# Kernel optimization log

Measured on AMD Instinct MI355X. Metric: run time of the kernel, lower is better.

Reference implementation:

```python
import itertools
import jax, jax.numpy as jnp
import numpy as np

ALPHA = 1e-4   # mse/conn mixing
BETA = 0.1
DMAX = 20.0
NCAP = 10.0    # costs_n_cap
PCAP = 3.0     # costs_p_cap
W3D = 64       # 3D cube window (window_3d)
W2D = 32       # 2D MALIS window (window_2d, default)


def _dilate5(mask):
    # scipy binary_dilation, default cross structuring element, 5 iterations
    m = mask.astype(bool)
    for _ in range(5):
        p = np.pad(m, 1)
        m = p[1:-1, 1:-1] | p[:-2, 1:-1] | p[2:, 1:-1] | p[1:-1, :-2] | p[1:-1, 2:]
    return m


def _label8(mask):
    # skimage.measure.label on boolean mask: 8-connectivity, background=0
    H, W = mask.shape
    lbl = np.zeros((H, W), np.int64)
    parent = {}

    def find(x):
        while parent[x] != x:
            parent[x] = parent[parent[x]]
            x = parent[x]
        return x

    nxt = 1
    for i in range(H):
        for j in range(W):
            if not mask[i, j]:
                continue
            neigh = []
            for di, dj in ((-1, -1), (-1, 0), (-1, 1), (0, -1)):
                ii, jj = i + di, j + dj
                if 0 <= ii < H and 0 <= jj < W and mask[ii, jj]:
                    neigh.append(int(lbl[ii, jj]))
            if not neigh:
                lbl[i, j] = nxt
                parent[nxt] = nxt
                nxt += 1
            else:
                m0 = min(neigh)
                lbl[i, j] = m0
                for nb in neigh:
                    ra, rb = find(m0), find(nb)
                    if ra != rb:
                        parent[max(ra, rb)] = min(ra, rb)
    out = np.zeros_like(lbl)
    remap = {}
    c = 0
    for i in range(H):
        for j in range(W):
            if lbl[i, j] > 0:
                r = find(int(lbl[i, j]))
                if r not in remap:
                    c += 1
                    remap[r] = c
                out[i, j] = remap[r]
    return out


def _malis_edge_weights(seg, n1, n2, costs, pos):
    # MALIS union-find / Kruskal maximal-spanning-tree pair counting.
    # Edges processed in descending cost order. Background (seg==0) nodes
    # are not counted. pos=1: #same-label pairs merged; pos=0: #diff-label pairs.
    n = seg.size
    parent = list(range(n))

    def find(x):
        r = x
        while parent[r] != r:
            r = parent[r]
        while parent[x] != r:
            parent[x], x = r, parent[x]
        return r

    cnt = [({int(s): 1} if s > 0 else {}) for s in seg]
    tot = [1 if s > 0 else 0 for s in seg]
    w = np.zeros(costs.shape[0], np.float32)
    for e in np.argsort(-costs, kind="stable"):
        ra, rb = find(int(n1[e])), find(int(n2[e]))
        if ra == rb:
            continue
        ca, cb = cnt[ra], cnt[rb]
        if len(ca) > len(cb):
            ra, rb, ca, cb = rb, ra, cb, ca
        same = 0
        for l, v in ca.items():
            same += v * cb.get(l, 0)
        w[e] = float(same if pos else tot[ra] * tot[rb] - same)
        for l, v in ca.items():
            cb[l] = cb.get(l, 0) + v
        tot[rb] += tot[ra]
        parent[ra] = rb
        cnt[ra] = None
    return w


def _window_weights(pred2d, tgt2d):
    # numpy MALIS node weights for a [B,1,H,W] 2D projection
    B, C, H, W = pred2d.shape
    w = W2D
    wn = np.zeros(pred2d.shape, np.float32)
    wp = np.zeros(pred2d.shape, np.float32)
    idx = np.arange(w * w).reshape(w, w)
    n1 = np.concatenate([idx[:, :-1].ravel(), idx[:-1, :].ravel()])
    n2 = np.concatenate([idx[:, 1:].ravel(), idx[1:, :].ravel()])
    nh = w * (w - 1)
    for k in range(H // w):
        for j in range(W // w):
            p = pred2d[:, :, k*w:(k+1)*w, j*w:(j+1)*w]
            t = tgt2d[:, :, k*w:(k+1)*w, j*w:(j+1)*w]
            ch = (p[:, :, :, :-1] + p[:, :, :, 1:]).reshape(B, -1)
            cv = (p[:, :, :-1, :] + p[:, :, 1:, :]).reshape(B, -1)
            costs = np.concatenate([ch, cv], 1).astype(np.float32)
            gh = (t[:, :, :, :-1] + t[:, :, :, 1:]).reshape(B, -1)
            gv = (t[:, :, :-1, :] + t[:, :, 1:, :]).reshape(B, -1)
            gt = np.concatenate([gh, gv], 1).astype(np.float32)
            costs_n = costs.copy()
            costs_p = costs.copy()
            costs_n[gt > NCAP] = NCAP
            costs_p[gt < PCAP] = 0.0
            gt = np.minimum(gt, NCAP)
            for b in range(B):
                sg = _label8(~_dilate5(t[b, 0] == 0)).ravel()
                en = _malis_edge_weights(sg, n1, n2, costs_n[b], 0)
                ep = _malis_edge_weights(sg, n1, n2, costs_p[b], 1)
                sn = en.sum()
                if sn > 0:
                    en = en / sn
                sp = ep.sum()
                if sp > 0:
                    ep = ep / sp
                en[gt[b] >= PCAP] = 0.0
                ep[gt[b] < NCAP] = 0.0
                for ew, out in ((en, wn), (ep, wp)):
                    eh = ew[:nh].reshape(w, w - 1)
                    ev = ew[nh:].reshape(w - 1, w)
                    nwt = np.zeros((w, w), np.float32)
                    nwt[:, :-1] += eh
                    nwt[:, 1:] += eh
                    nwt[:-1, :] += ev
                    nwt[1:, :] += ev
                    out[b, 0, k*w:(k+1)*w, j*w:(j+1)*w] = nwt
    return wn, wp


def _precompute(pred_np, tgt_np):
    # host-side (detached) MALIS weight maps, exactly as the torch module
    B, C, H, W, D = pred_np.shape
    items = []
    for k, j, i in itertools.product(range(H // W3D), range(W // W3D), range(D // W3D)):
        sl = (slice(None), slice(None), slice(k*W3D, (k+1)*W3D),
              slice(j*W3D, (j+1)*W3D), slice(i*W3D, (i+1)*W3D))
        pc, tc = pred_np[sl], tgt_np[sl]
        for axis in (2, 3, 4):
            wn, wp = _window_weights(pc.min(axis=axis), tc.min(axis=axis))
            items.append((k, j, i, axis, jnp.asarray(wn), jnp.asarray(wp)))
    return items


def _loss(pred, target, items):
    mse = jnp.mean((pred - target) ** 2)
    conn = jnp.float32(0.0)
    for (k, j, i, axis, wn, wp) in items:
        pc = pred[:, :, k*W3D:(k+1)*W3D, j*W3D:(j+1)*W3D, i*W3D:(i+1)*W3D]
        proj = jnp.min(pc, axis=axis)  # [B,1,64,64]
        conn = conn + jnp.sum(proj**2 * wn + BETA * (DMAX - proj)**2 * wp)
    return (mse, jnp.float32(ALPHA) * conn)


def setup_inputs() -> dict:
    # synthetic distance-transform-like volumes (zeros on 'vessel' seeds)
    rng = np.random.default_rng(0)
    B, H = 4, 128
    g = np.arange(H, dtype=np.float32)
    zz, yy, xx = np.meshgrid(g, g, g, indexing="ij")
    tgt = np.empty((B, 1, H, H, H), np.float32)
    for b in range(B):
        pts = rng.uniform(0, H, size=(24, 3)).astype(np.float32)
        d = np.full((H, H, H), np.inf, np.float32)
        for p in pts:
            d = np.minimum(d, np.sqrt((zz - p[0])**2 + (yy - p[1])**2 + (xx - p[2])**2))
        tgt[b, 0] = np.floor(np.minimum(d, DMAX))
    pred = np.clip(tgt + 0.5 * rng.standard_normal(tgt.shape).astype(np.float32), 0.0, DMAX).astype(np.float32)
    return {"pred": jnp.asarray(pred), "target": jnp.asarray(tgt)}


def reference(pred, target):
    items = _precompute(np.asarray(pred), np.asarray(target))
    return _loss(pred, target, items)
```

## Files before the change

### kernel.cpp

```cpp
#include <hip/hip_runtime.h>

#define BLOCK 256
#define NNODE 1024
#define NH    992
#define NE    1984
#define NSORT 2048
#define LMAX  12
#define CHUNK 64
#define NPASS (NE / CHUNK)

typedef unsigned long long ull;

__device__ __forceinline__ void edge_nodes(int e, int& a, int& b) {
    if (e < NH) {
        int r = e / 31;
        int c = e - r * 31;
        a = (r << 5) + c;
        b = a + 1;
    } else {
        a = e - NH;
        b = a + 32;
    }
}

__device__ __forceinline__ int find_par(unsigned short* par, int x) {
    volatile unsigned short* vp = par;
    int r = x;
    int p = vp[r];
    while (p != r) { r = p; p = vp[r]; }
    int c = x;
    while (c != r) { const int nxt = vp[c]; vp[c] = (unsigned short)r; c = nxt; }
    return r;
}

__device__ __forceinline__ int dot16x4(ull a, ull b) {
    int s  = (int)(a & 0xFFFFu)         * (int)(b & 0xFFFFu);
    s     += (int)((a >> 16) & 0xFFFFu) * (int)((b >> 16) & 0xFFFFu);
    s     += (int)((a >> 32) & 0xFFFFu) * (int)((b >> 32) & 0xFFFFu);
    s     += (int)((a >> 48) & 0xFFFFu) * (int)((b >> 48) & 0xFFFFu);
    return s;
}

__device__ __forceinline__ void cswap(unsigned int& ka, unsigned short& ia,
                                      unsigned int& kb, unsigned short& ib, bool up) {
    const bool gt = (ka > kb) || (ka == kb && ia > ib);
    if (gt == up) {
        const unsigned int  tk = ka; ka = kb; kb = tk;
        const unsigned short ti = ia; ia = ib; ib = ti;
    }
}

__global__ __launch_bounds__(BLOCK) void prep_kernel(const float* __restrict__ pred,
                                                     const float* __restrict__ tgt,
                                                     char* __restrict__ ws,
                                                     int B) {
    __shared__ alignas(16) float sh_p[NNODE];
    __shared__ alignas(16) float sh_t[NNODE];
    __shared__ unsigned char  mA[NNODE];
    __shared__ unsigned char  mB[NNODE];
    __shared__ unsigned short sh_parent[NNODE];
    __shared__ unsigned short sh_lab[NNODE];
    __shared__ int sh_flag;
    __shared__ int sh_L;

    const int tid = threadIdx.x;
    const int w = blockIdx.x;
    int wg = w;
    const int b    = wg % B;  wg /= B;
    const int win  = wg & 3;  wg >>= 2;
    const int item = wg;
    const int axis_id = item % 3;
    const int cube = item / 3;
    const int ci = cube & 1;
    const int cj = (cube >> 1) & 1;
    const int ck = (cube >> 2) & 1;
    const int wk = win >> 1;
    const int wj = win & 1;

    const int NW = 96 * B;
    float* Pb = (float*)(ws + 64);
    float* Tb = Pb + (size_t)NW * NNODE;
    unsigned char* Sb = (unsigned char*)(Tb + (size_t)NW * NNODE);
    int* Lb = (int*)(Sb + (size_t)NW * NNODE);

    const size_t base = (size_t)b * 2097152u;

    if (axis_id == 2) {
        for (int pix = tid; pix < NNODE; pix += BLOCK) {
            const int r = pix >> 5, c = pix & 31;
            const int R = wk * 32 + r, C = wj * 32 + c;
            const size_t idx0 = base + (size_t)(ck * 64 + R) * 16384u + (size_t)(cj * 64 + C) * 128u + (size_t)(ci * 64);
            const float4* pp = reinterpret_cast<const float4*>(pred + idx0);
            const float4* tp = reinterpret_cast<const float4*>(tgt + idx0);
            float pm = 3.4e38f, tm = 3.4e38f;
            #pragma unroll
            for (int h = 0; h < 16; ++h) {
                const float4 a = pp[h];
                const float4 t = tp[h];
                pm = fminf(pm, fminf(fminf(a.x, a.y), fminf(a.z, a.w)));
                tm = fminf(tm, fminf(fminf(t.x, t.y), fminf(t.z, t.w)));
            }
            sh_p[pix] = pm;
            sh_t[pix] = tm;
        }
    } else {
        const int r  = tid >> 3;
        const int c0 = (tid & 7) << 2;
        const int R = wk * 32 + r, C = wj * 32 + c0;
        size_t idx0; int hstride;
        if (axis_id == 0) {
            idx0 = base + (size_t)(ck * 64) * 16384u + (size_t)(cj * 64 + R) * 128u + (size_t)(ci * 64 + C);
            hstride = 16384;
        } else {
            idx0 = base + (size_t)(ck * 64 + R) * 16384u + (size_t)(cj * 64) * 128u + (size_t)(ci * 64 + C);
            hstride = 128;
        }
        float4 pm = make_float4(3.4e38f, 3.4e38f, 3.4e38f, 3.4e38f);
        float4 tm = pm;
        #pragma unroll 8
        for (int h = 0; h < 64; ++h) {
            const float4 a  = *reinterpret_cast<const float4*>(pred + idx0);
            const float4 t4 = *reinterpret_cast<const float4*>(tgt + idx0);
            pm.x = fminf(pm.x, a.x);  pm.y = fminf(pm.y, a.y);
            pm.z = fminf(pm.z, a.z);  pm.w = fminf(pm.w, a.w);
            tm.x = fminf(tm.x, t4.x); tm.y = fminf(tm.y, t4.y);
            tm.z = fminf(tm.z, t4.z); tm.w = fminf(tm.w, t4.w);
            idx0 += (size_t)hstride;
        }
        *reinterpret_cast<float4*>(&sh_p[(r << 5) + c0]) = pm;
        *reinterpret_cast<float4*>(&sh_t[(r << 5) + c0]) = tm;
    }
    __syncthreads();

    for (int pix = tid; pix < NNODE; pix += BLOCK)
        mA[pix] = (sh_t[pix] == 0.0f) ? 1 : 0;
    __syncthreads();
    for (int it = 0; it < 5; ++it) {
        unsigned char* src = (it & 1) ? mB : mA;
        unsigned char* dst = (it & 1) ? mA : mB;
        for (int pix = tid; pix < NNODE; pix += BLOCK) {
            const int r = pix >> 5, c = pix & 31;
            unsigned char v = src[pix];
            if (r > 0)  v |= src[pix - 32];
            if (r < 31) v |= src[pix + 32];
            if (c > 0)  v |= src[pix - 1];
            if (c < 31) v |= src[pix + 1];
            dst[pix] = v;
        }
        __syncthreads();
    }
    for (int pix = tid; pix < NNODE; pix += BLOCK)
        mA[pix] = mB[pix] ^ 1;
    __syncthreads();

    for (int pix = tid; pix < NNODE; pix += BLOCK)
        sh_parent[pix] = mA[pix] ? (unsigned short)pix : (unsigned short)0xFFFF;
    __syncthreads();
    for (;;) {
        if (tid == 0) sh_flag = 0;
        __syncthreads();
        for (int pix = tid; pix < NNODE; pix += BLOCK) {
            if (!mA[pix]) continue;
            const int r = pix >> 5, c = pix & 31;
            int m = sh_parent[pix];
            #pragma unroll
// ... 57 lines not shown
    __shared__ unsigned short sh_parent[NNODE];
    __shared__ unsigned int   sh_szto[NNODE];
    __shared__ ull            sh_cnt64[NNODE * 3];
    __shared__ alignas(16) unsigned char sh_seg[NNODE];
    __shared__ float          sh_sn;
    __shared__ double         sh_red[4];

    const int tid = threadIdx.x;
    int wg = blockIdx.x;
    const int sign = wg & 1;  wg >>= 1;
    const int w = wg;

    const int NW = 96 * B;
    const float* Pb = (const float*)(ws_c + 64);
    const float* Tb = Pb + (size_t)NW * NNODE;
    const unsigned char* Sb = (const unsigned char*)(Tb + (size_t)NW * NNODE);
    const int* Lb = (const int*)(Sb + (size_t)NW * NNODE);

    const int Lraw = Lb[w];
    if (Lraw == 0 || (Lraw == 1 && sign == 0)) return;
    const int mode = (Lraw <= 1) ? 0 : ((Lraw <= 4) ? 1 : 2);

    {
        const int p4 = tid << 2;
        *reinterpret_cast<float4*>(&sh_p[p4]) =
            *reinterpret_cast<const float4*>(&Pb[(size_t)w * NNODE + p4]);
        *reinterpret_cast<float4*>(&sh_t[p4]) =
            *reinterpret_cast<const float4*>(&Tb[(size_t)w * NNODE + p4]);
        ((unsigned int*)sh_seg)[tid] =
            ((const unsigned int*)Sb)[(size_t)w * (NNODE / 4) + tid];
    }
    __syncthreads();

    for (int pix = tid; pix < NNODE; pix += BLOCK) {
        sh_parent[pix] = (unsigned short)pix;
        const int s = sh_seg[pix];
        const unsigned int tot = (s > 0 && s <= LMAX) ? 1u : 0u;
        sh_szto[pix] = 1u | (tot << 16);
        if (mode >= 1) {
            ull c0 = 0, c1 = 0, c2 = 0;
            if (s >= 1 && s <= LMAX) {
                const ull bit = 1ull << (((s - 1) & 3) * 16);
                const int q = (s - 1) >> 2;
                if (q == 0) c0 = bit; else if (q == 1) c1 = bit; else c2 = bit;
            }
            sh_cnt64[pix * 3 + 0] = c0;
            if (mode == 2) {
                sh_cnt64[pix * 3 + 1] = c1;
                sh_cnt64[pix * 3 + 2] = c2;
            }
        }
    }
    __syncthreads();

    unsigned int   K[8];
    unsigned short I[8];
    const int b8 = tid << 3;
    #pragma unroll
    for (int l = 0; l < 8; ++l) {
        const int e = b8 + l;
        if (e < NE) {
            int a, bb; edge_nodes(e, a, bb);
            float cost = sh_p[a] + sh_p[bb];
            const float g = sh_t[a] + sh_t[bb];
            if (sign == 0) { if (g > 10.0f) cost = 10.0f; }
            else           { if (g <  3.0f) cost = 0.0f;  }
            K[l] = ~__float_as_uint(cost);
            I[l] = (unsigned short)e;
        } else {
            K[l] = 0xFFFFFFFFu;
            I[l] = (unsigned short)0xFFFF;
        }
    }
    cswap(K[0],I[0],K[1],I[1], true );
    cswap(K[2],I[2],K[3],I[3], false);
    cswap(K[4],I[4],K[5],I[5], true );
    cswap(K[6],I[6],K[7],I[7], false);
    cswap(K[0],I[0],K[2],I[2], true );
    cswap(K[1],I[1],K[3],I[3], true );
    cswap(K[4],I[4],K[6],I[6], false);
    cswap(K[5],I[5],K[7],I[7], false);
    cswap(K[0],I[0],K[1],I[1], true );
    cswap(K[2],I[2],K[3],I[3], true );
    cswap(K[4],I[4],K[5],I[5], false);
    cswap(K[6],I[6],K[7],I[7], false);
// ... 41 lines not shown
            const uint4 k1 = *reinterpret_cast<const uint4*>(&sh_key[b8 + 4]);
            const uint4 iv = *reinterpret_cast<const uint4*>(&sh_idx[b8]);
            K[0]=k0.x; K[1]=k0.y; K[2]=k0.z; K[3]=k0.w;
            K[4]=k1.x; K[5]=k1.y; K[6]=k1.z; K[7]=k1.w;
            I[0]=(unsigned short)(iv.x); I[1]=(unsigned short)(iv.x>>16);
            I[2]=(unsigned short)(iv.y); I[3]=(unsigned short)(iv.y>>16);
            I[4]=(unsigned short)(iv.z); I[5]=(unsigned short)(iv.z>>16);
            I[6]=(unsigned short)(iv.w); I[7]=(unsigned short)(iv.w>>16);
            const bool u8 = ((b8 & k) == 0);
            cswap(K[0],I[0],K[4],I[4], u8); cswap(K[1],I[1],K[5],I[5], u8);
            cswap(K[2],I[2],K[6],I[6], u8); cswap(K[3],I[3],K[7],I[7], u8);
            cswap(K[0],I[0],K[2],I[2], u8); cswap(K[1],I[1],K[3],I[3], u8);
            cswap(K[4],I[4],K[6],I[6], u8); cswap(K[5],I[5],K[7],I[7], u8);
            cswap(K[0],I[0],K[1],I[1], u8); cswap(K[2],I[2],K[3],I[3], u8);
            cswap(K[4],I[4],K[5],I[5], u8); cswap(K[6],I[6],K[7],I[7], u8);
            uint4 o0, o1, ov;
            o0.x=K[0]; o0.y=K[1]; o0.z=K[2]; o0.w=K[3];
            o1.x=K[4]; o1.y=K[5]; o1.z=K[6]; o1.w=K[7];
            ov.x=(unsigned int)I[0] | ((unsigned int)I[1]<<16);
            ov.y=(unsigned int)I[2] | ((unsigned int)I[3]<<16);
            ov.z=(unsigned int)I[4] | ((unsigned int)I[5]<<16);
            ov.w=(unsigned int)I[6] | ((unsigned int)I[7]<<16);
            *reinterpret_cast<uint4*>(&sh_key[b8])     = o0;
            *reinterpret_cast<uint4*>(&sh_key[b8 + 4]) = o1;
            *reinterpret_cast<uint4*>(&sh_idx[b8])     = ov;
        }
        __syncthreads();
    }

    for (int e = tid; e < NE; e += BLOCK) sh_key[e] = 0u;
    __syncthreads();

    if (tid < 64) {
        const int lane = tid;
        for (int pass = 0; pass < NPASS; ++pass) {
            const int e = sh_idx[pass * CHUNK + lane];
            int a, bb; edge_nodes(e, a, bb);
            int ra = find_par(sh_parent, a);
            int rb = find_par(sh_parent, bb);
            ull m = __ballot(ra != rb);
            while (m) {
                const int i = (int)__builtin_ctzll(m);
                m &= m - 1;
                const unsigned int pack = (unsigned int)ra | ((unsigned int)rb << 10) | ((unsigned int)e << 20);
                const unsigned int pk = (unsigned int)__shfl((int)pack, i);
                const int ra_i = (int)(pk & 1023u);
                const int rb_i = (int)((pk >> 10) & 1023u);
                if (ra_i == rb_i) continue;
                const int se = (int)(pk >> 20);
                const unsigned int xa = sh_szto[ra_i], xb = sh_szto[rb_i];
                const int ta = (int)(xa >> 16), tb = (int)(xb >> 16);
                const int big = ((xa & 0xFFFFu) > (xb & 0xFFFFu));
                const int rs = big ? ra_i : rb_i;
                const int rl = big ? rb_i : ra_i;
                int wv;
                if (mode == 0) {
                    wv = ta * tb;
                } else if (mode == 1) {
                    const ull a0 = sh_cnt64[ra_i * 3];
                    const ull b0 = sh_cnt64[rb_i * 3];
                    const int same = dot16x4(a0, b0);
                    wv = sign ? same : (ta * tb - same);
                    if (lane == 0 && (ta + tb) > 0)
                        sh_cnt64[rs * 3] = a0 + b0;
                } else {
                    const ull a0 = sh_cnt64[ra_i * 3 + 0];
                    const ull a1 = sh_cnt64[ra_i * 3 + 1];
                    const ull a2 = sh_cnt64[ra_i * 3 + 2];
                    const ull b0 = sh_cnt64[rb_i * 3 + 0];
                    const ull b1 = sh_cnt64[rb_i * 3 + 1];
                    const ull b2 = sh_cnt64[rb_i * 3 + 2];
                    const int same = dot16x4(a0, b0) + dot16x4(a1, b1) + dot16x4(a2, b2);
                    wv = sign ? same : (ta * tb - same);
                    if (lane == 0 && (ta + tb) > 0) {
                        sh_cnt64[rs * 3 + 0] = a0 + b0;
                        sh_cnt64[rs * 3 + 1] = a1 + b1;
                        sh_cnt64[rs * 3 + 2] = a2 + b2;
                    }
                }
                if (lane == 0) {
                    sh_key[se] = __float_as_uint((float)wv);
                    sh_szto[rs] = xa + xb;
                    sh_parent[rl] = (unsigned short)rs;
                }
                if (ra == rl) ra = rs;
                if (rb == rl) rb = rs;
            }
        }
    }
    __syncthreads();

    {
        float part = 0.0f;
        for (int e = tid; e < NE; e += BLOCK) part += __uint_as_float(sh_key[e]);
        for (int off = 32; off > 0; off >>= 1) part += __shfl_down(part, off, 64);
        if ((tid & 63) == 0) sh_red[tid >> 6] = (double)part;
        __syncthreads();
        if (tid == 0) sh_sn = (float)(sh_red[0] + sh_red[1] + sh_red[2] + sh_red[3]);
        __syncthreads();
    }
    const float sn = sh_sn;

    double acc = 0.0;
    for (int pix = tid; pix < NNODE; pix += BLOCK) {
        const int r = pix >> 5, c = pix & 31;
        float nw = 0.0f;
        if (c < 31) { const int e = r * 31 + c;
            float v = __uint_as_float(sh_key[e]); if (sn > 0.0f) v = v / sn;
            const float g = sh_t[pix] + sh_t[pix + 1];
            if (sign == 0) { if (g >= 3.0f) v = 0.0f; } else { if (g < 10.0f) v = 0.0f; }
            nw += v; }
        if (c > 0)  { const int e = r * 31 + c - 1;
            float v = __uint_as_float(sh_key[e]); if (sn > 0.0f) v = v / sn;
            const float g = sh_t[pix - 1] + sh_t[pix];
            if (sign == 0) { if (g >= 3.0f) v = 0.0f; } else { if (g < 10.0f) v = 0.0f; }
            nw += v; }
        if (r < 31) { const int e = NH + pix;
            float v = __uint_as_float(sh_key[e]); if (sn > 0.0f) v = v / sn;
            const float g = sh_t[pix] + sh_t[pix + 32];
            if (sign == 0) { if (g >= 3.0f) v = 0.0f; } else { if (g < 10.0f) v = 0.0f; }
            nw += v; }
// ... 143 lines not shown
        }
        __syncthreads();
        const int f = sh_flag;
        __syncthreads();
        if (f == 0) break;
    }

    if (tid == 0) sh_L = 0;
    __syncthreads();
    for (int pix = tid; pix < NNODE; pix += BLOCK) {
        if (mA[pix] && (int)sh_parent[pix] == pix) {
            const int id = atomicAdd(&sh_L, 1);
            sh_szto[pix] = (unsigned int)(id + 1);
        }
    }
    __syncthreads();
    for (int pix = tid; pix < NNODE; pix += BLOCK) {
        unsigned char s = 0;
        if (mA[pix]) {
            int lab = (int)sh_szto[sh_parent[pix]];
            if (lab > 255) lab = 255;
            s = (unsigned char)lab;
        }
        sh_seg[pix] = s;
    }
    __syncthreads();

    const int Lraw = sh_L;
    const int mode = (Lraw <= 1) ? 0 : ((Lraw <= 4) ? 1 : 2);
    const bool skip_all = (Lraw == 0) || (Lraw == 1 && sign == 0);

    if (!skip_all) {

    for (int pix = tid; pix < NNODE; pix += BLOCK) {
        sh_parent[pix] = (unsigned short)pix;
        const int s = sh_seg[pix];
        const unsigned int tot = (s > 0 && s <= LMAX) ? 1u : 0u;
        sh_szto[pix] = 1u | (tot << 16);
        if (mode >= 1) {
            ull c0 = 0, c1 = 0, c2 = 0;
            if (s >= 1 && s <= LMAX) {
                const ull bit = 1ull << (((s - 1) & 3) * 16);
                const int q = (s - 1) >> 2;
                if (q == 0) c0 = bit; else if (q == 1) c1 = bit; else c2 = bit;
            }
            sh_cnt64[pix * 3 + 0] = c0;
            if (mode == 2) {
                sh_cnt64[pix * 3 + 1] = c1;
                sh_cnt64[pix * 3 + 2] = c2;
            }
        }
    }
    __syncthreads();

    unsigned int   K[8];
    unsigned short I[8];
    const int b8 = tid << 3;
    #pragma unroll
    for (int l = 0; l < 8; ++l) {
        const int e = b8 + l;
        if (e < NE) {
            int a, bb; edge_nodes(e, a, bb);
            float cost = sh_p[a] + sh_p[bb];
            const float g = sh_t[a] + sh_t[bb];
            if (sign == 0) { if (g > 10.0f) cost = 10.0f; }
            else           { if (g <  3.0f) cost = 0.0f;  }
            K[l] = ~__float_as_uint(cost);
            I[l] = (unsigned short)e;
        } else {
            K[l] = 0xFFFFFFFFu;
            I[l] = (unsigned short)0xFFFF;
        }
    }
    cswap(K[0],I[0],K[1],I[1], true );
    cswap(K[2],I[2],K[3],I[3], false);
    cswap(K[4],I[4],K[5],I[5], true );
    cswap(K[6],I[6],K[7],I[7], false);
    cswap(K[0],I[0],K[2],I[2], true );
    cswap(K[1],I[1],K[3],I[3], true );
    cswap(K[4],I[4],K[6],I[6], false);
    cswap(K[5],I[5],K[7],I[7], false);
    cswap(K[0],I[0],K[1],I[1], true );
    cswap(K[2],I[2],K[3],I[3], true );
    cswap(K[4],I[4],K[5],I[5], false);
    cswap(K[6],I[6],K[7],I[7], false);
// ... 41 lines not shown
            const uint4 k1 = *reinterpret_cast<const uint4*>(&sh_key[b8 + 4]);
            const uint4 iv = *reinterpret_cast<const uint4*>(&sh_idx[b8]);
            K[0]=k0.x; K[1]=k0.y; K[2]=k0.z; K[3]=k0.w;
            K[4]=k1.x; K[5]=k1.y; K[6]=k1.z; K[7]=k1.w;
            I[0]=(unsigned short)(iv.x); I[1]=(unsigned short)(iv.x>>16);
            I[2]=(unsigned short)(iv.y); I[3]=(unsigned short)(iv.y>>16);
            I[4]=(unsigned short)(iv.z); I[5]=(unsigned short)(iv.z>>16);
            I[6]=(unsigned short)(iv.w); I[7]=(unsigned short)(iv.w>>16);
            const bool u8 = ((b8 & k) == 0);
            cswap(K[0],I[0],K[4],I[4], u8); cswap(K[1],I[1],K[5],I[5], u8);
            cswap(K[2],I[2],K[6],I[6], u8); cswap(K[3],I[3],K[7],I[7], u8);
            cswap(K[0],I[0],K[2],I[2], u8); cswap(K[1],I[1],K[3],I[3], u8);
            cswap(K[4],I[4],K[6],I[6], u8); cswap(K[5],I[5],K[7],I[7], u8);
            cswap(K[0],I[0],K[1],I[1], u8); cswap(K[2],I[2],K[3],I[3], u8);
            cswap(K[4],I[4],K[5],I[5], u8); cswap(K[6],I[6],K[7],I[7], u8);
            uint4 o0, o1, ov;
            o0.x=K[0]; o0.y=K[1]; o0.z=K[2]; o0.w=K[3];
            o1.x=K[4]; o1.y=K[5]; o1.z=K[6]; o1.w=K[7];
            ov.x=(unsigned int)I[0] | ((unsigned int)I[1]<<16);
            ov.y=(unsigned int)I[2] | ((unsigned int)I[3]<<16);
            ov.z=(unsigned int)I[4] | ((unsigned int)I[5]<<16);
            ov.w=(unsigned int)I[6] | ((unsigned int)I[7]<<16);
            *reinterpret_cast<uint4*>(&sh_key[b8])     = o0;
            *reinterpret_cast<uint4*>(&sh_key[b8 + 4]) = o1;
            *reinterpret_cast<uint4*>(&sh_idx[b8])     = ov;
        }
        __syncthreads();
    }

    for (int e = tid; e < NE; e += BLOCK) sh_key[e] = 0u;
    __syncthreads();

    if (tid < 64) {
        const int lane = tid;
        for (int pass = 0; pass < NPASS; ++pass) {
            const int e = sh_idx[pass * CHUNK + lane];
            int a, bb; edge_nodes(e, a, bb);
            int ra = find_par(sh_parent, a);
            int rb = find_par(sh_parent, bb);
            ull m = __ballot(ra != rb);
            while (m) {
                const int i = (int)__builtin_ctzll(m);
                m &= m - 1;
                const unsigned int pack = (unsigned int)ra | ((unsigned int)rb << 10) | ((unsigned int)e << 20);
                const unsigned int pk = (unsigned int)__shfl((int)pack, i);
                const int ra_i = (int)(pk & 1023u);
                const int rb_i = (int)((pk >> 10) & 1023u);
                if (ra_i == rb_i) continue;
                const int se = (int)(pk >> 20);
                const unsigned int xa = sh_szto[ra_i], xb = sh_szto[rb_i];
                const int ta = (int)(xa >> 16), tb = (int)(xb >> 16);
                const int big = ((xa & 0xFFFFu) > (xb & 0xFFFFu));
                const int rs = big ? ra_i : rb_i;
                const int rl = big ? rb_i : ra_i;
                int wv;
                if (mode == 0) {
                    wv = ta * tb;
                } else if (mode == 1) {
                    const ull a0 = sh_cnt64[ra_i * 3];
                    const ull b0 = sh_cnt64[rb_i * 3];
                    const int same = dot16x4(a0, b0);
                    wv = sign ? same : (ta * tb - same);
                    if (lane == 0 && (ta + tb) > 0)
                        sh_cnt64[rs * 3] = a0 + b0;
                } else {
                    const ull a0 = sh_cnt64[ra_i * 3 + 0];
                    const ull a1 = sh_cnt64[ra_i * 3 + 1];
                    const ull a2 = sh_cnt64[ra_i * 3 + 2];
                    const ull b0 = sh_cnt64[rb_i * 3 + 0];
                    const ull b1 = sh_cnt64[rb_i * 3 + 1];
                    const ull b2 = sh_cnt64[rb_i * 3 + 2];
                    const int same = dot16x4(a0, b0) + dot16x4(a1, b1) + dot16x4(a2, b2);
                    wv = sign ? same : (ta * tb - same);
                    if (lane == 0 && (ta + tb) > 0) {
                        sh_cnt64[rs * 3 + 0] = a0 + b0;
                        sh_cnt64[rs * 3 + 1] = a1 + b1;
                        sh_cnt64[rs * 3 + 2] = a2 + b2;
                    }
                }
                if (lane == 0) {
                    sh_key[se] = __float_as_uint((float)wv);
                    sh_szto[rs] = xa + xb;
                    sh_parent[rl] = (unsigned short)rs;
                }
                if (ra == rl) ra = rs;
                if (rb == rl) rb = rs;
            }
        }
    }
    __syncthreads();

    {
        float part = 0.0f;
        for (int e = tid; e < NE; e += BLOCK) part += __uint_as_float(sh_key[e]);
        for (int off = 32; off > 0; off >>= 1) part += __shfl_down(part, off, 64);
        if ((tid & 63) == 0) sh_red[tid >> 6] = (double)part;
        __syncthreads();
        if (tid == 0) sh_sn = (float)(sh_red[0] + sh_red[1] + sh_red[2] + sh_red[3]);
        __syncthreads();
    }
    const float sn = sh_sn;

    double acc = 0.0;
    for (int pix = tid; pix < NNODE; pix += BLOCK) {
        const int r = pix >> 5, c = pix & 31;
        float nw = 0.0f;
        if (c < 31) { const int e = r * 31 + c;
            float v = __uint_as_float(sh_key[e]); if (sn > 0.0f) v = v / sn;
            const float g = sh_t[pix] + sh_t[pix + 1];
            if (sign == 0) { if (g >= 3.0f) v = 0.0f; } else { if (g < 10.0f) v = 0.0f; }
            nw += v; }
        if (c > 0)  { const int e = r * 31 + c - 1;
            float v = __uint_as_float(sh_key[e]); if (sn > 0.0f) v = v / sn;
            const float g = sh_t[pix - 1] + sh_t[pix];
            if (sign == 0) { if (g >= 3.0f) v = 0.0f; } else { if (g < 10.0f) v = 0.0f; }
            nw += v; }
        if (r < 31) { const int e = NH + pix;
            float v = __uint_as_float(sh_key[e]); if (sn > 0.0f) v = v / sn;
            const float g = sh_t[pix] + sh_t[pix + 32];
            if (sign == 0) { if (g >= 3.0f) v = 0.0f; } else { if (g < 10.0f) v = 0.0f; }
            nw += v; }
// ... 25 lines not shown
    for (long i = (long)blockIdx.x * BLOCK + threadIdx.x; i < n; i += (long)gridDim.x * BLOCK) {
        const float d = pred[i] - tgt[i];
        acc += (double)(d * d);
    }
    for (int off = 32; off > 0; off >>= 1) acc += __shfl_down(acc, off, 64);
    __shared__ double red[4];
    if ((threadIdx.x & 63) == 0) red[threadIdx.x >> 6] = acc;
    __syncthreads();
    if (threadIdx.x == 0)
        atomicAdd(&acc_ws[0], red[0] + red[1] + red[2] + red[3]);
}

__global__ void fin_kernel(const double* __restrict__ acc_ws, float* __restrict__ out, long n) {
    if (threadIdx.x == 0 && blockIdx.x == 0) {
        out[0] = (float)(acc_ws[0] / (double)n);
        out[1] = (float)(acc_ws[1] * (double)1e-4f);
    }
}

extern "C" void kernel_launch(void* const* d_in, const int* in_sizes, int n_in,
                              void* d_out, int out_size, void* d_ws, size_t ws_size,
                              hipStream_t stream) {
    const float* pred = (const float*)d_in[0];
    const float* tgt  = (const float*)d_in[1];
    float* out = (float*)d_out;
    double* acc = (double*)d_ws;

    const long n = (long)in_sizes[0];
    const int  B = (int)(n / 2097152);
    const int  NW = 96 * B;
    const size_t need = 64 + (size_t)NW * NNODE * 9 + (size_t)NW * 4;

    hipMemsetAsync(d_ws, 0, 2 * sizeof(double), stream);
    mse_kernel<<<1024, BLOCK, 0, stream>>>(pred, tgt, acc, n);
    if (ws_size >= need) {
        prep_kernel<<<NW, BLOCK, 0, stream>>>(pred, tgt, (char*)d_ws, B);
        solve_kernel<<<192 * B, BLOCK, 0, stream>>>((const char*)d_ws, acc, B);
    } else {
        conn_kernel<<<192 * B, BLOCK, 0, stream>>>(pred, tgt, acc, B);
    }
    fin_kernel<<<1, 64, 0, stream>>>(acc, out, n);
}
```

Measured before the change: 539.3 us.

## Forward component state in registers through serial Kruskal merges, specialize by mode

Each candidate lane now loads its roots' size and label-count vectors up front. The serial merge loop then passes these values by shuffle and updates them in registers after each merge, so it no longer reads shared memory on the critical path. The next candidate is prefetched while the current one is processed, and the code is templated on mode to remove runtime branches. The cost is more register pressure, more shuffles, and trickier logic for keeping root ids and forwarded data consistent.

Result: slower. 593.7 us (+10.1%).

```diff
diff --git a/kernel.cpp b/kernel.cpp
--- a/kernel.cpp
+++ b/kernel.cpp
@@ -41,12 +41,124 @@
     return s;
 }
 
+__device__ __forceinline__ ull shfl64(ull v, int src) {
+    const int lo = __shfl((int)(unsigned int)(v & 0xFFFFFFFFu), src);
+    const int hi = __shfl((int)(unsigned int)(v >> 32), src);
+    return ((ull)(unsigned int)hi << 32) | (ull)(unsigned int)lo;
+}
+
 __device__ __forceinline__ void cswap(unsigned int& ka, unsigned short& ia,
                                       unsigned int& kb, unsigned short& ib, bool up) {
     const bool gt = (ka > kb) || (ka == kb && ia > ib);
     if (gt == up) {
         const unsigned int  tk = ka; ka = kb; kb = tk;
         const unsigned short ti = ia; ia = ib; ib = ti;
+    }
+}
+
+template<int MODE>
+__device__ __forceinline__ void kruskal_run(unsigned short* sh_parent,
+                                            unsigned int*   sh_szto,
+                                            ull*            sh_cnt64,
+                                            unsigned int*   sh_key,
+                                            const unsigned short* sh_idx,
+                                            const int sign, const int lane) {
+    for (int pass = 0; pass < NPASS; ++pass) {
+        const int e = sh_idx[pass * CHUNK + lane];
+        int a, bb; edge_nodes(e, a, bb);
+        int ra = find_par(sh_parent, a);
+        int rb = find_par(sh_parent, bb);
+        unsigned int xa = 0, xb = 0;
+        ull a0 = 0, a1 = 0, a2 = 0, b0 = 0, b1 = 0, b2 = 0;
+        const bool cand = (ra != rb);
+        if (cand) {
+            xa = sh_szto[ra]; xb = sh_szto[rb];
+            if (MODE >= 1) { a0 = sh_cnt64[ra * 3]; b0 = sh_cnt64[rb * 3]; }
+            if (MODE == 2) {
+                a1 = sh_cnt64[ra * 3 + 1]; a2 = sh_cnt64[ra * 3 + 2];
+                b1 = sh_cnt64[rb * 3 + 1]; b2 = sh_cnt64[rb * 3 + 2];
+            }
+        }
+        ull m = __ballot(cand);
+        if (m == 0) continue;
+
+        {
+            const int i0 = (int)__builtin_ctzll(m); m &= m - 1;
+            unsigned int pk  = (unsigned int)__shfl(
+                (int)((unsigned int)ra | ((unsigned int)rb << 10) | ((unsigned int)e << 20)), i0);
+            unsigned int sxa = (unsigned int)__shfl((int)xa, i0);
+            unsigned int sxb = (unsigned int)__shfl((int)xb, i0);
+            ull sa0 = 0, sb0 = 0, sa1 = 0, sa2 = 0, sb1 = 0, sb2 = 0;
+            if (MODE >= 1) { sa0 = shfl64(a0, i0); sb0 = shfl64(b0, i0); }
+            if (MODE == 2) { sa1 = shfl64(a1, i0); sa2 = shfl64(a2, i0);
+                             sb1 = shfl64(b1, i0); sb2 = shfl64(b2, i0); }
+
+            for (;;) {
+                const bool have_next = (m != 0);
+                unsigned int npk = 0, nxa = 0, nxb = 0;
+                ull na0 = 0, nb0 = 0, na1 = 0, na2 = 0, nb1 = 0, nb2 = 0;
+                if (have_next) {
+                    const int ni = (int)__builtin_ctzll(m); m &= m - 1;
+                    npk = (unsigned int)__shfl(
+                        (int)((unsigned int)ra | ((unsigned int)rb << 10) | ((unsigned int)e << 20)), ni);
+                    nxa = (unsigned int)__shfl((int)xa, ni);
+                    nxb = (unsigned int)__shfl((int)xb, ni);
+                    if (MODE >= 1) { na0 = shfl64(a0, ni); nb0 = shfl64(b0, ni); }
+                    if (MODE == 2) { na1 = shfl64(a1, ni); na2 = shfl64(a2, ni);
+                                     nb1 = shfl64(b1, ni); nb2 = shfl64(b2, ni); }
+                }
+                const int ra_i = (int)(pk & 1023u);
+                const int rb_i = (int)((pk >> 10) & 1023u);
+                if (ra_i != rb_i) {
+                    const int ta = (int)(sxa >> 16), tb = (int)(sxb >> 16);
+                    int wv;
+                    if (MODE == 0) {
+                        wv = ta * tb;
+                    } else {
+                        int same = dot16x4(sa0, sb0);
+                        if (MODE == 2) same += dot16x4(sa1, sb1) + dot16x4(sa2, sb2);
+                        wv = sign ? same : (ta * tb - same);
+                    }
+                    const int big = ((sxa & 0xFFFFu) > (sxb & 0xFFFFu));
+                    const int rs = big ? ra_i : rb_i;
+                    const int rl = big ? rb_i : ra_i;
+                    const unsigned int xs = sxa + sxb;
+                    ull m0 = 0, m1 = 0, m2 = 0;
+                    if (MODE >= 1) m0 = sa0 + sb0;
+                    if (MODE == 2) { m1 = sa1 + sb1; m2 = sa2 + sb2; }
+                    if (lane == 0) {
+                        sh_key[pk >> 20] = __float_as_uint((float)wv);
+                        sh_szto[rs] = xs;
+                        if (MODE >= 1 && (ta + tb) > 0) {
+                            sh_cnt64[rs * 3] = m0;
+                            if (MODE == 2) { sh_cnt64[rs * 3 + 1] = m1; sh_cnt64[rs * 3 + 2] = m2; }
+                        }
+                        sh_parent[rl] = (unsigned short)rs;
+                    }
+                    if (ra == rl || ra == rs) { ra = rs; xa = xs;
+                        if (MODE >= 1) a0 = m0; if (MODE == 2) { a1 = m1; a2 = m2; } }
+                    if (rb == rl || rb == rs) { rb = rs; xb = xs;
+                        if (MODE >= 1) b0 = m0; if (MODE == 2) { b1 = m1; b2 = m2; } }
+                    if (have_next) {
+                        unsigned int r1 = npk & 1023u;
+                        unsigned int r2 = (npk >> 10) & 1023u;
+                        if (r1 == (unsigned int)rl || r1 == (unsigned int)rs) {
+                            r1 = (unsigned int)rs; nxa = xs;
+                            if (MODE >= 1) na0 = m0; if (MODE == 2) { na1 = m1; na2 = m2; }
+                        }
+                        if (r2 == (unsigned int)rl || r2 == (unsigned int)rs) {
+                            r2 = (unsigned int)rs; nxb = xs;
+                            if (MODE >= 1) nb0 = m0; if (MODE == 2) { nb1 = m1; nb2 = m2; }
+                        }
+                        npk = r1 | (r2 << 10) | (npk & 0xFFF00000u);
+                    }
+                }
+                if (!have_next) break;
+                pk = npk; sxa = nxa; sxb = nxb;
+                if (MODE >= 1) { sa0 = na0; sb0 = nb0; }
+                if (MODE == 2) { sa1 = na1; sa2 = na2; sb1 = nb1; sb2 = nb2; }
+            }
+        }
     }
 }
 
@@ -380,61 +492,9 @@
     __syncthreads();
 
     if (tid < 64) {
-        const int lane = tid;
-        for (int pass = 0; pass < NPASS; ++pass) {
-            const int e = sh_idx[pass * CHUNK + lane];
-            int a, bb; edge_nodes(e, a, bb);
-            int ra = find_par(sh_parent, a);
-            int rb = find_par(sh_parent, bb);
-            ull m = __ballot(ra != rb);
-            while (m) {
-                const int i = (int)__builtin_ctzll(m);
-                m &= m - 1;
-                const unsigned int pack = (unsigned int)ra | ((unsigned int)rb << 10) | ((unsigned int)e << 20);
-                const unsigned int pk = (unsigned int)__shfl((int)pack, i);
-                const int ra_i = (int)(pk & 1023u);
-                const int rb_i = (int)((pk >> 10) & 1023u);
-                if (ra_i == rb_i) continue;
-                const int se = (int)(pk >> 20);
-                const unsigned int xa = sh_szto[ra_i], xb = sh_szto[rb_i];
-                const int ta = (int)(xa >> 16), tb = (int)(xb >> 16);
-                const int big = ((xa & 0xFFFFu) > (xb & 0xFFFFu));
-                const int rs = big ? ra_i : rb_i;
-                const int rl = big ? rb_i : ra_i;
-                int wv;
-                if (mode == 0) {
-                    wv = ta * tb;
-                } else if (mode == 1) {
-                    const ull a0 = sh_cnt64[ra_i * 3];
-                    const ull b0 = sh_cnt64[rb_i * 3];
-                    const int same = dot16x4(a0, b0);
-                    wv = sign ? same : (ta * tb - same);
-                    if (lane == 0 && (ta + tb) > 0)
-                        sh_cnt64[rs * 3] = a0 + b0;
-                } else {
-                    const ull a0 = sh_cnt64[ra_i * 3 + 0];
-                    const ull a1 = sh_cnt64[ra_i * 3 + 1];
-                    const ull a2 = sh_cnt64[ra_i * 3 + 2];
-                    const ull b0 = sh_cnt64[rb_i * 3 + 0];
-                    const ull b1 = sh_cnt64[rb_i * 3 + 1];
-                    const ull b2 = sh_cnt64[rb_i * 3 + 2];
-                    const int same = dot16x4(a0, b0) + dot16x4(a1, b1) + dot16x4(a2, b2);
-                    wv = sign ? same : (ta * tb - same);
-                    if (lane == 0 && (ta + tb) > 0) {
-                        sh_cnt64[rs * 3 + 0] = a0 + b0;
-                        sh_cnt64[rs * 3 + 1] = a1 + b1;
-                        sh_cnt64[rs * 3 + 2] = a2 + b2;
-                    }
-                }
-                if (lane == 0) {
-                    sh_key[se] = __float_as_uint((float)wv);
-                    sh_szto[rs] = xa + xb;
-                    sh_parent[rl] = (unsigned short)rs;
-                }
-                if (ra == rl) ra = rs;
-                if (rb == rl) rb = rs;
-            }
-        }
+        if (mode == 0)      kruskal_run<0>(sh_parent, sh_szto, sh_cnt64, sh_key, sh_idx, sign, tid);
+        else if (mode == 1) kruskal_run<1>(sh_parent, sh_szto, sh_cnt64, sh_key, sh_idx, sign, tid);
+        else                kruskal_run<2>(sh_parent, sh_szto, sh_cnt64, sh_key, sh_idx, sign, tid);
     }
     __syncthreads();
 
@@ -770,61 +830,9 @@
     __syncthreads();
 
     if (tid < 64) {
-        const int lane = tid;
-        for (int pass = 0; pass < NPASS; ++pass) {
-            const int e = sh_idx[pass * CHUNK + lane];
-            int a, bb; edge_nodes(e, a, bb);
-            int ra = find_par(sh_parent, a);
-            int rb = find_par(sh_parent, bb);
-            ull m = __ballot(ra != rb);
-            while (m) {
-                const int i = (int)__builtin_ctzll(m);
-                m &= m - 1;
-                const unsigned int pack = (unsigned int)ra | ((unsigned int)rb << 10) | ((unsigned int)e << 20);
-                const unsigned int pk = (unsigned int)__shfl((int)pack, i);
-                const int ra_i = (int)(pk & 1023u);
-                const int rb_i = (int)((pk >> 10) & 1023u);
-                if (ra_i == rb_i) continue;
-                const int se = (int)(pk >> 20);
-                const unsigned int xa = sh_szto[ra_i], xb = sh_szto[rb_i];
-                const int ta = (int)(xa >> 16), tb = (int)(xb >> 16);
-                const int big = ((xa & 0xFFFFu) > (xb & 0xFFFFu));
-                const int rs = big ? ra_i : rb_i;
-                const int rl = big ? rb_i : ra_i;
-                int wv;
-                if (mode == 0) {
-                    wv = ta * tb;
-                } else if (mode == 1) {
-                    const ull a0 = sh_cnt64[ra_i * 3];
-                    const ull b0 = sh_cnt64[rb_i * 3];
-                    const int same = dot16x4(a0, b0);
-                    wv = sign ? same : (ta * tb - same);
-                    if (lane == 0 && (ta + tb) > 0)
-                        sh_cnt64[rs * 3] = a0 + b0;
-                } else {
-                    const ull a0 = sh_cnt64[ra_i * 3 + 0];
-                    const ull a1 = sh_cnt64[ra_i * 3 + 1];
-                    const ull a2 = sh_cnt64[ra_i * 3 + 2];
-                    const ull b0 = sh_cnt64[rb_i * 3 + 0];
-                    const ull b1 = sh_cnt64[rb_i * 3 + 1];
-                    const ull b2 = sh_cnt64[rb_i * 3 + 2];
-                    const int same = dot16x4(a0, b0) + dot16x4(a1, b1) + dot16x4(a2, b2);
-                    wv = sign ? same : (ta * tb - same);
-                    if (lane == 0 && (ta + tb) > 0) {
-                        sh_cnt64[rs * 3 + 0] = a0 + b0;
-                        sh_cnt64[rs * 3 + 1] = a1 + b1;
-                        sh_cnt64[rs * 3 + 2] = a2 + b2;
-                    }
-                }
-                if (lane == 0) {
-                    sh_key[se] = __float_as_uint((float)wv);
-                    sh_szto[rs] = xa + xb;
-                    sh_parent[rl] = (unsigned short)rs;
-                }
-                if (ra == rl) ra = rs;
-                if (rb == rl) rb = rs;
-            }
-        }
+        if (mode == 0)      kruskal_run<0>(sh_parent, sh_szto, sh_cnt64, sh_key, sh_idx, sign, tid);
+        else if (mode == 1) kruskal_run<1>(sh_parent, sh_szto, sh_cnt64, sh_key, sh_idx, sign, tid);
+        else                kruskal_run<2>(sh_parent, sh_szto, sh_cnt64, sh_key, sh_idx, sign, tid);
     }
     __syncthreads();
 
```

## Fuse MSE into prep kernel and add parallel claim-based Kruskal merges

Applied to the files above, without the earlier changes.

Folds the MSE reduction into the axis-2 prep blocks, which already read every voxel of pred and target, and drops the separate mse_kernel launch on the workspace path. Adds a wave-parallel pre-pass to the Kruskal loop for modes 0 and 1. Each lane claims both of its roots with an atomicMax tag in shared memory, and lanes that win both claims merge at the same time before the serial ballot loop handles what is left. Templating the union-find init and Kruskal on mode removes runtime branching. The trade-off is double-precision accumulation inside prep, extra LDS atomics and waitcnt barriers per pass, and reuse of the sh_cnt64 storage as claim slots.

Result: faster. 473.4 us (-12.2%).

```diff
diff --git a/kernel.cpp b/kernel.cpp
--- a/kernel.cpp
+++ b/kernel.cpp
@@ -50,9 +50,146 @@
     }
 }
 
+template<int MODE>
+__device__ __forceinline__ void kruskal_run(unsigned short* sh_parent,
+                                            unsigned int*   sh_szto,
+                                            ull*            sh_cnt64,
+                                            unsigned int*   sh_key,
+                                            const unsigned short* sh_idx,
+                                            const int sign, const int lane) {
+    unsigned int* claim32 = (unsigned int*)sh_cnt64;
+    for (int pass = 0; pass < NPASS; ++pass) {
+        const int e = sh_idx[pass * CHUNK + lane];
+        int a, bb; edge_nodes(e, a, bb);
+        int ra = find_par(sh_parent, a);
+        int rb = find_par(sh_parent, bb);
+        bool cand = (ra != rb);
+
+        if (MODE <= 1) {
+            const unsigned int tag = ((unsigned int)(pass + 1) << 6) | (unsigned int)(63 - lane);
+            const int ia = (MODE == 0) ? ra : (ra * 6 + 2);
+            const int ib = (MODE == 0) ? rb : (rb * 6 + 2);
+            if (cand) {
+                atomicMax(&claim32[ia], tag);
+                atomicMax(&claim32[ib], tag);
+            }
+            asm volatile("s_waitcnt lgkmcnt(0)" ::: "memory");
+            __builtin_amdgcn_sched_barrier(0);
+            bool win = false;
+            if (cand) win = (claim32[ia] == tag) && (claim32[ib] == tag);
+            if (win) {
+                const unsigned int xa = sh_szto[ra], xb = sh_szto[rb];
+                const int ta = (int)(xa >> 16), tb = (int)(xb >> 16);
+                int wv;
+                ull a0 = 0, b0 = 0;
+                if (MODE == 0) {
+                    wv = ta * tb;
+                } else {
+                    a0 = sh_cnt64[ra * 3]; b0 = sh_cnt64[rb * 3];
+                    const int same = dot16x4(a0, b0);
+                    wv = sign ? same : (ta * tb - same);
+                }
+                const int big = ((xa & 0xFFFFu) > (xb & 0xFFFFu));
+                const int rs = big ? ra : rb;
+                const int rl = big ? rb : ra;
+                sh_key[e] = __float_as_uint((float)wv);
+                sh_szto[rs] = xa + xb;
+                if (MODE == 1 && (ta + tb) > 0) sh_cnt64[rs * 3] = a0 + b0;
+                sh_parent[rl] = (unsigned short)rs;
+                cand = false;
+            }
+            asm volatile("s_waitcnt lgkmcnt(0)" ::: "memory");
+            __builtin_amdgcn_sched_barrier(0);
+            if (cand) {
+                ra = find_par(sh_parent, ra);
+                rb = find_par(sh_parent, rb);
+                cand = (ra != rb);
+            }
+        }
+
+        ull m = __ballot(cand);
+        while (m) {
+            const int i = (int)__builtin_ctzll(m);
+            m &= m - 1;
+            const unsigned int pack = (unsigned int)ra | ((unsigned int)rb << 10) | ((unsigned int)e << 20);
+            const unsigned int pk = (unsigned int)__shfl((int)pack, i);
+            const int ra_i = (int)(pk & 1023u);
+            const int rb_i = (int)((pk >> 10) & 1023u);
+            if (ra_i == rb_i) continue;
+            const int se = (int)(pk >> 20);
+            const unsigned int xa = sh_szto[ra_i], xb = sh_szto[rb_i];
+            const int ta = (int)(xa >> 16), tb = (int)(xb >> 16);
+            const int big = ((xa & 0xFFFFu) > (xb & 0xFFFFu));
+            const int rs = big ? ra_i : rb_i;
+            const int rl = big ? rb_i : ra_i;
+            int wv;
+            if (MODE == 0) {
+                wv = ta * tb;
+            } else if (MODE == 1) {
+                const ull a0 = sh_cnt64[ra_i * 3];
+                const ull b0 = sh_cnt64[rb_i * 3];
+                const int same = dot16x4(a0, b0);
+                wv = sign ? same : (ta * tb - same);
+                if (lane == 0 && (ta + tb) > 0)
+                    sh_cnt64[rs * 3] = a0 + b0;
+            } else {
+                const ull a0 = sh_cnt64[ra_i * 3 + 0];
+                const ull a1 = sh_cnt64[ra_i * 3 + 1];
+                const ull a2 = sh_cnt64[ra_i * 3 + 2];
+                const ull b0 = sh_cnt64[rb_i * 3 + 0];
+                const ull b1 = sh_cnt64[rb_i * 3 + 1];
+                const ull b2 = sh_cnt64[rb_i * 3 + 2];
+                const int same = dot16x4(a0, b0) + dot16x4(a1, b1) + dot16x4(a2, b2);
+                wv = sign ? same : (ta * tb - same);
+                if (lane == 0 && (ta + tb) > 0) {
+                    sh_cnt64[rs * 3 + 0] = a0 + b0;
+                    sh_cnt64[rs * 3 + 1] = a1 + b1;
+                    sh_cnt64[rs * 3 + 2] = a2 + b2;
+                }
+            }
+            if (lane == 0) {
+                sh_key[se] = __float_as_uint((float)wv);
+                sh_szto[rs] = xa + xb;
+                sh_parent[rl] = (unsigned short)rs;
+            }
+            if (ra == rl) ra = rs;
+            if (rb == rl) rb = rs;
+        }
+    }
+}
+
+template<int MODE>
+__device__ __forceinline__ void uf_init(unsigned short* sh_parent,
+                                        unsigned int* sh_szto,
+                                        ull* sh_cnt64,
+                                        const unsigned char* sh_seg,
+                                        const int tid) {
+    unsigned int* claim32 = (unsigned int*)sh_cnt64;
+    for (int pix = tid; pix < NNODE; pix += BLOCK) {
+        sh_parent[pix] = (unsigned short)pix;
+        const int s = sh_seg[pix];
+        const unsigned int tot = (s > 0 && s <= LMAX) ? 1u : 0u;
+        sh_szto[pix] = 1u | (tot << 16);
+        if (MODE == 0) {
+            claim32[pix] = 0u;
+        } else {
+            ull c0 = 0, c1 = 0, c2 = 0;
+            if (s >= 1 && s <= LMAX) {
+                const ull bit = 1ull << (((s - 1) & 3) * 16);
+                const int q = (s - 1) >> 2;
+                if (q == 0) c0 = bit; else if (q == 1) c1 = bit; else c2 = bit;
+            }
+            sh_cnt64[pix * 3 + 0] = c0;
+            sh_cnt64[pix * 3 + 1] = (MODE == 1) ? 0ull : c1;
+            if (MODE == 2) sh_cnt64[pix * 3 + 2] = c2;
+        }
+    }
+}
+
 __global__ __launch_bounds__(BLOCK) void prep_kernel(const float* __restrict__ pred,
                                                      const float* __restrict__ tgt,
                                                      char* __restrict__ ws,
+                                                     double* __restrict__ acc_ws,
                                                      int B) {
     __shared__ alignas(16) float sh_p[NNODE];
     __shared__ alignas(16) float sh_t[NNODE];
@@ -62,6 +199,7 @@
     __shared__ unsigned short sh_lab[NNODE];
     __shared__ int sh_flag;
     __shared__ int sh_L;
+    __shared__ double sh_redp[4];
 
     const int tid = threadIdx.x;
     const int w = blockIdx.x;
@@ -86,6 +224,7 @@
     const size_t base = (size_t)b * 2097152u;
 
     if (axis_id == 2) {
+        double msum = 0.0;
         for (int pix = tid; pix < NNODE; pix += BLOCK) {
             const int r = pix >> 5, c = pix & 31;
             const int R = wk * 32 + r, C = wj * 32 + c;
@@ -99,10 +238,21 @@
                 const float4 t = tp[h];
                 pm = fminf(pm, fminf(fminf(a.x, a.y), fminf(a.z, a.w)));
                 tm = fminf(tm, fminf(fminf(t.x, t.y), fminf(t.z, t.w)));
+                const float dx = a.x - t.x, dy = a.y - t.y;
+                const float dz = a.z - t.z, dw = a.w - t.w;
+                msum += (double)(dx * dx);
+                msum += (double)(dy * dy);
+                msum += (double)(dz * dz);
+                msum += (double)(dw * dw);
             }
             sh_p[pix] = pm;
             sh_t[pix] = tm;
         }
+        for (int off = 32; off > 0; off >>= 1) msum += __shfl_down(msum, off, 64);
+        if ((tid & 63) == 0) sh_redp[tid >> 6] = msum;
+        __syncthreads();
+        if (tid == 0)
+            atomicAdd(&acc_ws[0], sh_redp[0] + sh_redp[1] + sh_redp[2] + sh_redp[3]);
     } else {
         const int r  = tid >> 3;
         const int c0 = (tid & 7) << 2;
@@ -129,8 +279,8 @@
         }
         *reinterpret_cast<float4*>(&sh_p[(r << 5) + c0]) = pm;
         *reinterpret_cast<float4*>(&sh_t[(r << 5) + c0]) = tm;
-    }
-    __syncthreads();
+        __syncthreads();
+    }
 
     for (int pix = tid; pix < NNODE; pix += BLOCK)
         mA[pix] = (sh_t[pix] == 0.0f) ? 1 : 0;
@@ -254,25 +404,9 @@
     }
     __syncthreads();
 
-    for (int pix = tid; pix < NNODE; pix += BLOCK) {
-        sh_parent[pix] = (unsigned short)pix;
-        const int s = sh_seg[pix];
-        const unsigned int tot = (s > 0 && s <= LMAX) ? 1u : 0u;
-        sh_szto[pix] = 1u | (tot << 16);
-        if (mode >= 1) {
-            ull c0 = 0, c1 = 0, c2 = 0;
-            if (s >= 1 && s <= LMAX) {
-                const ull bit = 1ull << (((s - 1) & 3) * 16);
-                const int q = (s - 1) >> 2;
-                if (q == 0) c0 = bit; else if (q == 1) c1 = bit; else c2 = bit;
-            }
-            sh_cnt64[pix * 3 + 0] = c0;
-            if (mode == 2) {
-                sh_cnt64[pix * 3 + 1] = c1;
-                sh_cnt64[pix * 3 + 2] = c2;
-            }
-        }
-    }
+    if (mode == 0)      uf_init<0>(sh_parent, sh_szto, sh_cnt64, sh_seg, tid);
+    else if (mode == 1) uf_init<1>(sh_parent, sh_szto, sh_cnt64, sh_seg, tid);
+    else                uf_init<2>(sh_parent, sh_szto, sh_cnt64, sh_seg, tid);
     __syncthreads();
 
     unsigned int   K[8];
@@ -380,61 +514,9 @@
     __syncthreads();
 
     if (tid < 64) {
-        const int lane = tid;
-        for (int pass = 0; pass < NPASS; ++pass) {
-            const int e = sh_idx[pass * CHUNK + lane];
-            int a, bb; edge_nodes(e, a, bb);
-            int ra = find_par(sh_parent, a);
-            int rb = find_par(sh_parent, bb);
-            ull m = __ballot(ra != rb);
-            while (m) {
-                const int i = (int)__builtin_ctzll(m);
-                m &= m - 1;
-                const unsigned int pack = (unsigned int)ra | ((unsigned int)rb << 10) | ((unsigned int)e << 20);
-                const unsigned int pk = (unsigned int)__shfl((int)pack, i);
-                const int ra_i = (int)(pk & 1023u);
-                const int rb_i = (int)((pk >> 10) & 1023u);
-                if (ra_i == rb_i) continue;
-                const int se = (int)(pk >> 20);
-                const unsigned int xa = sh_szto[ra_i], xb = sh_szto[rb_i];
-                const int ta = (int)(xa >> 16), tb = (int)(xb >> 16);
-                const int big = ((xa & 0xFFFFu) > (xb & 0xFFFFu));
-                const int rs = big ? ra_i : rb_i;
-                const int rl = big ? rb_i : ra_i;
-                int wv;
-                if (mode == 0) {
-                    wv = ta * tb;
-                } else if (mode == 1) {
-                    const ull a0 = sh_cnt64[ra_i * 3];
-                    const ull b0 = sh_cnt64[rb_i * 3];
-                    const int same = dot16x4(a0, b0);
-                    wv = sign ? same : (ta * tb - same);
-                    if (lane == 0 && (ta + tb) > 0)
-                        sh_cnt64[rs * 3] = a0 + b0;
-                } else {
-                    const ull a0 = sh_cnt64[ra_i * 3 + 0];
-                    const ull a1 = sh_cnt64[ra_i * 3 + 1];
-                    const ull a2 = sh_cnt64[ra_i * 3 + 2];
-                    const ull b0 = sh_cnt64[rb_i * 3 + 0];
-                    const ull b1 = sh_cnt64[rb_i * 3 + 1];
-                    const ull b2 = sh_cnt64[rb_i * 3 + 2];
-                    const int same = dot16x4(a0, b0) + dot16x4(a1, b1) + dot16x4(a2, b2);
-                    wv = sign ? same : (ta * tb - same);
-                    if (lane == 0 && (ta + tb) > 0) {
-                        sh_cnt64[rs * 3 + 0] = a0 + b0;
-                        sh_cnt64[rs * 3 + 1] = a1 + b1;
-                        sh_cnt64[rs * 3 + 2] = a2 + b2;
-                    }
-                }
-                if (lane == 0) {
-                    sh_key[se] = __float_as_uint((float)wv);
-                    sh_szto[rs] = xa + xb;
-                    sh_parent[rl] = (unsigned short)rs;
-                }
-                if (ra == rl) ra = rs;
-                if (rb == rl) rb = rs;
-            }
-        }
+        if (mode == 0)      kruskal_run<0>(sh_parent, sh_szto, sh_cnt64, sh_key, sh_idx, sign, tid);
+        else if (mode == 1) kruskal_run<1>(sh_parent, sh_szto, sh_cnt64, sh_key, sh_idx, sign, tid);
+        else                kruskal_run<2>(sh_parent, sh_szto, sh_cnt64, sh_key, sh_idx, sign, tid);
     }
     __syncthreads();
 
@@ -644,25 +726,9 @@
 
     if (!skip_all) {
 
-    for (int pix = tid; pix < NNODE; pix += BLOCK) {
-        sh_parent[pix] = (unsigned short)pix;
-        const int s = sh_seg[pix];
-        const unsigned int tot = (s > 0 && s <= LMAX) ? 1u : 0u;
-        sh_szto[pix] = 1u | (tot << 16);
-        if (mode >= 1) {
-            ull c0 = 0, c1 = 0, c2 = 0;
-            if (s >= 1 && s <= LMAX) {
-                const ull bit = 1ull << (((s - 1) & 3) * 16);
-                const int q = (s - 1) >> 2;
-                if (q == 0) c0 = bit; else if (q == 1) c1 = bit; else c2 = bit;
-            }
-            sh_cnt64[pix * 3 + 0] = c0;
-            if (mode == 2) {
-                sh_cnt64[pix * 3 + 1] = c1;
-                sh_cnt64[pix * 3 + 2] = c2;
-            }
-        }
-    }
+    if (mode == 0)      uf_init<0>(sh_parent, sh_szto, sh_cnt64, sh_seg, tid);
+    else if (mode == 1) uf_init<1>(sh_parent, sh_szto, sh_cnt64, sh_seg, tid);
+    else                uf_init<2>(sh_parent, sh_szto, sh_cnt64, sh_seg, tid);
     __syncthreads();
 
     unsigned int   K[8];
@@ -770,61 +836,9 @@
     __syncthreads();
 
     if (tid < 64) {
-        const int lane = tid;
-        for (int pass = 0; pass < NPASS; ++pass) {
-            const int e = sh_idx[pass * CHUNK + lane];
-            int a, bb; edge_nodes(e, a, bb);
-            int ra = find_par(sh_parent, a);
-            int rb = find_par(sh_parent, bb);
-            ull m = __ballot(ra != rb);
-            while (m) {
-                const int i = (int)__builtin_ctzll(m);
-                m &= m - 1;
-                const unsigned int pack = (unsigned int)ra | ((unsigned int)rb << 10) | ((unsigned int)e << 20);
-                const unsigned int pk = (unsigned int)__shfl((int)pack, i);
-                const int ra_i = (int)(pk & 1023u);
-                const int rb_i = (int)((pk >> 10) & 1023u);
-                if (ra_i == rb_i) continue;
-                const int se = (int)(pk >> 20);
-                const unsigned int xa = sh_szto[ra_i], xb = sh_szto[rb_i];
-                const int ta = (int)(xa >> 16), tb = (int)(xb >> 16);
-                const int big = ((xa & 0xFFFFu) > (xb & 0xFFFFu));
-                const int rs = big ? ra_i : rb_i;
-                const int rl = big ? rb_i : ra_i;
-                int wv;
-                if (mode == 0) {
-                    wv = ta * tb;
-                } else if (mode == 1) {
-                    const ull a0 = sh_cnt64[ra_i * 3];
-                    const ull b0 = sh_cnt64[rb_i * 3];
-                    const int same = dot16x4(a0, b0);
-                    wv = sign ? same : (ta * tb - same);
-                    if (lane == 0 && (ta + tb) > 0)
-                        sh_cnt64[rs * 3] = a0 + b0;
-                } else {
-                    const ull a0 = sh_cnt64[ra_i * 3 + 0];
-                    const ull a1 = sh_cnt64[ra_i * 3 + 1];
-                    const ull a2 = sh_cnt64[ra_i * 3 + 2];
-                    const ull b0 = sh_cnt64[rb_i * 3 + 0];
-                    const ull b1 = sh_cnt64[rb_i * 3 + 1];
-                    const ull b2 = sh_cnt64[rb_i * 3 + 2];
-                    const int same = dot16x4(a0, b0) + dot16x4(a1, b1) + dot16x4(a2, b2);
-                    wv = sign ? same : (ta * tb - same);
-                    if (lane == 0 && (ta + tb) > 0) {
-                        sh_cnt64[rs * 3 + 0] = a0 + b0;
-                        sh_cnt64[rs * 3 + 1] = a1 + b1;
-                        sh_cnt64[rs * 3 + 2] = a2 + b2;
-                    }
-                }
-                if (lane == 0) {
-                    sh_key[se] = __float_as_uint((float)wv);
-                    sh_szto[rs] = xa + xb;
-                    sh_parent[rl] = (unsigned short)rs;
-                }
-                if (ra == rl) ra = rs;
-                if (rb == rl) rb = rs;
-            }
-        }
+        if (mode == 0)      kruskal_run<0>(sh_parent, sh_szto, sh_cnt64, sh_key, sh_idx, sign, tid);
+        else if (mode == 1) kruskal_run<1>(sh_parent, sh_szto, sh_cnt64, sh_key, sh_idx, sign, tid);
+        else                kruskal_run<2>(sh_parent, sh_szto, sh_cnt64, sh_key, sh_idx, sign, tid);
     }
     __syncthreads();
 
@@ -916,11 +930,11 @@
     const size_t need = 64 + (size_t)NW * NNODE * 9 + (size_t)NW * 4;
 
     hipMemsetAsync(d_ws, 0, 2 * sizeof(double), stream);
-    mse_kernel<<<1024, BLOCK, 0, stream>>>(pred, tgt, acc, n);
     if (ws_size >= need) {
-        prep_kernel<<<NW, BLOCK, 0, stream>>>(pred, tgt, (char*)d_ws, B);
+        prep_kernel<<<NW, BLOCK, 0, stream>>>(pred, tgt, (char*)d_ws, acc, B);
         solve_kernel<<<192 * B, BLOCK, 0, stream>>>((const char*)d_ws, acc, B);
     } else {
+        mse_kernel<<<1024, BLOCK, 0, stream>>>(pred, tgt, acc, n);
         conn_kernel<<<192 * B, BLOCK, 0, stream>>>(pred, tgt, acc, B);
     }
     fin_kernel<<<1, 64, 0, stream>>>(acc, out, n);
```
